# Kernel optimization log

Hardware: AMD Instinct MI355X
Metric: run time of the kernel (lower is better)

Reference implementation:

```python
import jax, jax.numpy as jnp
import numpy as np


def setup_inputs() -> dict:
    key = jax.random.key(0)
    k1, k2 = jax.random.split(key)
    b, c, h, w = 2, 128, 96, 128
    feature0 = jax.random.normal(k1, (b, c, h, w), dtype=jnp.float32)
    feature1 = jax.random.normal(k2, (b, c, h, w), dtype=jnp.float32)
    return {"feature0": feature0, "feature1": feature1, "local_radius": 4}


def reference(feature0, feature1, local_radius):
    # Faithful to the torch module: sample coords are base pixel coords + integer
    # window offsets, so align_corners=True bilinear grid_sample with zeros padding
    # reduces exactly to an integer gather with out-of-bounds masking.
    b, c, h, w = feature0.shape
    r = int(local_radius)
    # base pixel coords (x, y), matching coords_grid channel order
    ys, xs = jnp.meshgrid(jnp.arange(h, dtype=jnp.float32),
                          jnp.arange(w, dtype=jnp.float32), indexing='ij')  # [h,w]
    # window offsets; row-major over (dy, dx) like generate_window_grid reshape(-1,2)
    dy, dx = jnp.meshgrid(jnp.arange(-r, r + 1), jnp.arange(-r, r + 1), indexing='ij')
    dy = dy.reshape(-1).astype(jnp.float32)  # [K]
    dx = dx.reshape(-1).astype(jnp.float32)
    K = dx.shape[0]

    sample_x = xs[:, :, None] + dx  # [h,w,K]
    sample_y = ys[:, :, None] + dy
    valid = ((sample_x >= 0) & (sample_x <= w - 1) &
             (sample_y >= 0) & (sample_y <= h - 1))  # [h,w,K]

    cxi = jnp.clip(sample_x, 0, w - 1).astype(jnp.int32)
    cyi = jnp.clip(sample_y, 0, h - 1).astype(jnp.int32)
    # gather: [b,c,h,w,K]; zeros padding outside bounds
    window_feature = feature1[:, :, cyi, cxi] * valid.astype(feature1.dtype)

    # correlation: per-pixel [1,c] x [c,K]
    corr = jnp.einsum('bchw,bchwk->bhwk', feature0, window_feature) / (c ** 0.5)
    prob = jax.nn.softmax(corr, axis=-1)  # [b,h,w,K]

    # weighted coord sum -> correspondence, then flow = correspondence - coords
    corr_x = jnp.sum(prob * sample_x, axis=-1)  # [b,h,w]
    corr_y = jnp.sum(prob * sample_y, axis=-1)
    flow = jnp.stack([corr_x - xs, corr_y - ys], axis=1)  # [b,2,h,w]

    match_prob = prob.reshape(b, h * w, K)
    return flow, match_prob
```

## Files before the change

kernel.cpp:

```cpp
#include <hip/hip_runtime.h>
#include <math.h>

#define W_ 128
#define H_ 96
#define C_ 128
#define HW_ (H_ * W_)
#define K_ 81
#define FLOW_ELEMS (2 * 2 * H_ * W_)
#define TCOLS 80
#define TSTR 66

typedef __fp16 f16x8 __attribute__((ext_vector_type(8)));
typedef float  f32x4 __attribute__((ext_vector_type(4)));

__device__ __forceinline__ unsigned pack_pair(float a, float b) {
    return __builtin_bit_cast(unsigned, __builtin_amdgcn_cvt_pkrtz(a, b));
}

__global__ __launch_bounds__(256) void fused_kernel(const float* __restrict__ f0,
                                                    const float* __restrict__ f1,
                                                    float* __restrict__ out) {
    __shared__ unsigned tile[TCOLS * TSTR];
    __shared__ float corr_lds[64][85];
    __shared__ float mbuf[64], ibuf[64];
    __shared__ float pmax[4][68], psum[4][68], pfxb[4][68], pfyb[4][68];

    const int t = threadIdx.x;
    const int wid = t >> 6, l = t & 63;
    const int L = (blockIdx.x & 7) * 48 + (blockIdx.x >> 3);
    const int xh = L & 1;
    const int y0 = (L >> 1) % H_;
    const int b  = L / (2 * H_);
    const int px0 = xh * 64 + wid * 16;

    int g_off[5], lds_w[5];
    bool g_ok[5];
#pragma unroll
    for (int i = 0; i < 5; ++i) {
        const int s = i * 256 + t;
        const int cp = s / 20;
        const int q = s - cp * 20;
        const int x0 = xh * 64 + 4 * q - 4;
        g_ok[i] = (x0 >= 0) && (x0 <= 124);
        g_off[i] = 2 * cp * HW_ + (g_ok[i] ? x0 : 0);
        lds_w[i] = (4 * q) * TSTR + cp;
    }
    const float* f1base = f1 + (size_t)b * C_ * HW_;

    f16x8 a[4];
    {
        const float* f0p = f0 + (size_t)b * C_ * HW_ + (size_t)y0 * W_ + px0 + (l & 15);
#pragma unroll
        for (int kk = 0; kk < 4; ++kk) {
            f16x8 av;
#pragma unroll
            for (int j = 0; j < 8; ++j)
                av[j] = (__fp16)f0p[(size_t)(kk * 32 + (l >> 4) * 8 + j) * HW_];
            a[kk] = av;
        }
    }

    auto LOADDY = [&](int dy, float4 (&va)[5], float4 (&vb)[5], bool& ok) {
        const int r = y0 + dy - 4;
        ok = (r >= 0) && (r < H_);
        const float* f1b = f1base + (size_t)(ok ? r : 0) * W_;
#pragma unroll
        for (int i = 0; i < 5; ++i) {
            float4 x = {0.f, 0.f, 0.f, 0.f}, y = {0.f, 0.f, 0.f, 0.f};
            if (ok && g_ok[i]) {
                x = *(const float4*)(f1b + g_off[i]);
                y = *(const float4*)(f1b + g_off[i] + HW_);
            }
            va[i] = x; vb[i] = y;
        }
    };
    auto WRITEDY = [&](const float4 (&va)[5], const float4 (&vb)[5]) {
#pragma unroll
        for (int i = 0; i < 5; ++i) {
            tile[lds_w[i]]            = pack_pair(va[i].x, vb[i].x);
            tile[lds_w[i] + TSTR]     = pack_pair(va[i].y, vb[i].y);
            tile[lds_w[i] + 2 * TSTR] = pack_pair(va[i].z, vb[i].z);
            tile[lds_w[i] + 3 * TSTR] = pack_pair(va[i].w, vb[i].w);
        }
    };
    auto COMPUTE = [&](int dy) {
        f32x4 accA = {0.f, 0.f, 0.f, 0.f}, accB = {0.f, 0.f, 0.f, 0.f};
#pragma unroll
        for (int kk = 0; kk < 4; ++kk) {
            const int off = kk * 16 + (l >> 4) * 4;
            {
                const int col = wid * 16 + (l & 15);
                const uint2 lo = *(const uint2*)&tile[col * TSTR + off];
                const uint2 hi = *(const uint2*)&tile[col * TSTR + off + 2];
                const uint4 u = {lo.x, lo.y, hi.x, hi.y};
                accA = __builtin_amdgcn_mfma_f32_16x16x32_f16(
                    a[kk], __builtin_bit_cast(f16x8, u), accA, 0, 0, 0);
            }
            {
                const int col = wid * 16 + 16 + (l & 15);
                const uint2 lo = *(const uint2*)&tile[col * TSTR + off];
                const uint2 hi = *(const uint2*)&tile[col * TSTR + off + 2];
                const uint4 u = {lo.x, lo.y, hi.x, hi.y};
                accB = __builtin_amdgcn_mfma_f32_16x16x32_f16(
                    a[kk], __builtin_bit_cast(f16x8, u), accB, 0, 0, 0);
            }
        }
#pragma unroll
        for (int h = 0; h < 2; ++h) {
            const f32x4 acc = h ? accB : accA;
#pragma unroll
            for (int rg = 0; rg < 4; ++rg) {
                const int i2 = (l >> 4) * 4 + rg;
                const int j2 = h * 16 + (l & 15);
                const int dxw = j2 - i2;
                if (dxw >= 0 && dxw <= 8)
                    corr_lds[wid * 16 + i2][dy * 9 + dxw] = acc[rg];
            }
        }
    };

    float4 vaA[5], vbA[5], vaB[5], vbB[5], vaC[5], vbC[5];
    bool okA, okB, okC;

    LOADDY(0, vaA, vbA, okA);
    LOADDY(1, vaB, vbB, okB);
    for (int i = t; i < 64 * 85; i += 256) (&corr_lds[0][0])[i] = 0.f;
    __syncthreads();

    if (okA) WRITEDY(vaA, vbA); __syncthreads();
    LOADDY(2, vaC, vbC, okC);
    if (okA) COMPUTE(0); __syncthreads();

    if (okB) WRITEDY(vaB, vbB); __syncthreads();
    LOADDY(3, vaA, vbA, okA);
    if (okB) COMPUTE(1); __syncthreads();

    if (okC) WRITEDY(vaC, vbC); __syncthreads();
    LOADDY(4, vaB, vbB, okB);
    if (okC) COMPUTE(2); __syncthreads();

    if (okA) WRITEDY(vaA, vbA); __syncthreads();
    LOADDY(5, vaC, vbC, okC);
    if (okA) COMPUTE(3); __syncthreads();

    if (okB) WRITEDY(vaB, vbB); __syncthreads();
    LOADDY(6, vaA, vbA, okA);
    if (okB) COMPUTE(4); __syncthreads();

    if (okC) WRITEDY(vaC, vbC); __syncthreads();
    LOADDY(7, vaB, vbB, okB);
    if (okC) COMPUTE(5); __syncthreads();

    if (okA) WRITEDY(vaA, vbA); __syncthreads();
    LOADDY(8, vaC, vbC, okC);
    if (okA) COMPUTE(6); __syncthreads();

    if (okB) WRITEDY(vaB, vbB); __syncthreads();
    if (okB) COMPUTE(7); __syncthreads();

    if (okC) WRITEDY(vaC, vbC); __syncthreads();
    if (okC) COMPUTE(8); __syncthreads();

    const float scale = 0.08838834764831845f;

    {
        const int px = t & 63;
        const int part = t >> 6;
        float pm = -1e30f;
        for (int k = part; k < K_; k += 4)
            pm = fmaxf(pm, corr_lds[px][k] * scale);
        pmax[part][px] = pm;
        __syncthreads();
        const float m = fmaxf(fmaxf(pmax[0][px], pmax[1][px]),
                              fmaxf(pmax[2][px], pmax[3][px]));
        float ps = 0.f, pfx = 0.f, pfy = 0.f;
        for (int k = part; k < K_; k += 4) {
            const float e = __expf(corr_lds[px][k] * scale - m);
            ps += e;
            pfx += e * (float)(k % 9 - 4);
            pfy += e * (float)(k / 9 - 4);
        }
        psum[part][px] = ps; pfxb[part][px] = pfx; pfyb[part][px] = pfy;
        __syncthreads();
        if (t < 64) {
            const float s = psum[0][t] + psum[1][t] + psum[2][t] + psum[3][t];
            const float inv = 1.f / s;
            mbuf[t] = m;
            ibuf[t] = inv;
            const float fx = pfxb[0][t] + pfxb[1][t] + pfxb[2][t] + pfxb[3][t];
            const float fy = pfyb[0][t] + pfyb[1][t] + pfyb[2][t] + pfyb[3][t];
            const int x = xh * 64 + t;
            out[((size_t)(b * 2 + 0) * H_ + y0) * W_ + x] = fx * inv;
            out[((size_t)(b * 2 + 1) * H_ + y0) * W_ + x] = fy * inv;
        }
    }
    __syncthreads();

    float* mp = out + FLOW_ELEMS + ((size_t)b * HW_ + (size_t)y0 * W_ + xh * 64) * K_;
    for (int f = t; f < 64 * K_; f += 256) {
        const int px = f / K_;
        const int k = f - px * K_;
        mp[f] = __expf(corr_lds[px][k] * scale - mbuf[px]) * ibuf[px];
    }
}

extern "C" void kernel_launch(void* const* d_in, const int* in_sizes, int n_in,
                              void* d_out, int out_size, void* d_ws, size_t ws_size,
                              hipStream_t stream) {
    (void)in_sizes; (void)n_in; (void)out_size; (void)d_ws; (void)ws_size;
    const float* f0 = (const float*)d_in[0];
    const float* f1 = (const float*)d_in[1];
    float* out = (float*)d_out;

    fused_kernel<<<384, 256, 0, stream>>>(f0, f1, out);
}
```

Baseline: 27.48 us.

## Split channel reduction across waves with LDS atomics, shrinking pixel tile to 16

Each block now covers 16 pixels instead of 64, and the four waves each take a 32-channel slice of the reduction instead of separate 16-pixel groups. Partial correlations are combined with LDS atomicAdd. The launch grows from 384 to 1536 blocks. The goal is more blocks in flight and a smaller per-block LDS footprint, but each block re-reads an overlapping 24-column f1 halo, uses smaller loads, and pays for shared-memory atomics.

```diff
diff --git a/kernel.cpp b/kernel.cpp
--- a/kernel.cpp
+++ b/kernel.cpp
@@ -7,7 +7,6 @@
 #define HW_ (H_ * W_)
 #define K_ 81
 #define FLOW_ELEMS (2 * 2 * H_ * W_)
-#define TCOLS 80
 #define TSTR 66
 
 typedef __fp16 f16x8 __attribute__((ext_vector_type(8)));
@@ -20,52 +19,48 @@
 __global__ __launch_bounds__(256) void fused_kernel(const float* __restrict__ f0,
                                                     const float* __restrict__ f1,
                                                     float* __restrict__ out) {
-    __shared__ unsigned tile[TCOLS * TSTR];
-    __shared__ float corr_lds[64][85];
-    __shared__ float mbuf[64], ibuf[64];
-    __shared__ float pmax[4][68], psum[4][68], pfxb[4][68], pfyb[4][68];
+    __shared__ unsigned tile[32 * TSTR];
+    __shared__ float corr_lds[16][85];
+    __shared__ float mbuf[16], ibuf[16];
+    __shared__ float pmax[16][17], psum[16][17], pfxb[16][17], pfyb[16][17];
 
     const int t = threadIdx.x;
     const int wid = t >> 6, l = t & 63;
-    const int L = (blockIdx.x & 7) * 48 + (blockIdx.x >> 3);
-    const int xh = L & 1;
-    const int y0 = (L >> 1) % H_;
-    const int b  = L / (2 * H_);
-    const int px0 = xh * 64 + wid * 16;
-
-    int g_off[5], lds_w[5];
-    bool g_ok[5];
-#pragma unroll
-    for (int i = 0; i < 5; ++i) {
+    const int L = (blockIdx.x & 7) * 192 + (blockIdx.x >> 3);
+    const int b = L / 768;
+    const int rem = L - b * 768;
+    const int y0 = rem >> 3;
+    const int xq = rem & 7;
+    const int px0 = xq * 16;
+
+    int g_off[2], lds_w[2];
+    bool g_ok[2];
+#pragma unroll
+    for (int i = 0; i < 2; ++i) {
         const int s = i * 256 + t;
-        const int cp = s / 20;
-        const int q = s - cp * 20;
-        const int x0 = xh * 64 + 4 * q - 4;
+        const int cp = s >> 3;
+        const int q = s & 7;
+        const int x0 = px0 + 4 * q - 4;
         g_ok[i] = (x0 >= 0) && (x0 <= 124);
         g_off[i] = 2 * cp * HW_ + (g_ok[i] ? x0 : 0);
         lds_w[i] = (4 * q) * TSTR + cp;
     }
     const float* f1base = f1 + (size_t)b * C_ * HW_;
 
-    f16x8 a[4];
+    f16x8 a;
     {
         const float* f0p = f0 + (size_t)b * C_ * HW_ + (size_t)y0 * W_ + px0 + (l & 15);
 #pragma unroll
-        for (int kk = 0; kk < 4; ++kk) {
-            f16x8 av;
-#pragma unroll
-            for (int j = 0; j < 8; ++j)
-                av[j] = (__fp16)f0p[(size_t)(kk * 32 + (l >> 4) * 8 + j) * HW_];
-            a[kk] = av;
-        }
-    }
-
-    auto LOADDY = [&](int dy, float4 (&va)[5], float4 (&vb)[5], bool& ok) {
+        for (int j = 0; j < 8; ++j)
+            a[j] = (__fp16)f0p[(size_t)(wid * 32 + (l >> 4) * 8 + j) * HW_];
+    }
+
+    auto LOADDY = [&](int dy, float4 (&va)[2], float4 (&vb)[2], bool& ok) {
         const int r = y0 + dy - 4;
         ok = (r >= 0) && (r < H_);
         const float* f1b = f1base + (size_t)(ok ? r : 0) * W_;
 #pragma unroll
-        for (int i = 0; i < 5; ++i) {
+        for (int i = 0; i < 2; ++i) {
             float4 x = {0.f, 0.f, 0.f, 0.f}, y = {0.f, 0.f, 0.f, 0.f};
             if (ok && g_ok[i]) {
                 x = *(const float4*)(f1b + g_off[i]);
@@ -74,9 +69,9 @@
             va[i] = x; vb[i] = y;
         }
     };
-    auto WRITEDY = [&](const float4 (&va)[5], const float4 (&vb)[5]) {
-#pragma unroll
-        for (int i = 0; i < 5; ++i) {
+    auto WRITEDY = [&](const float4 (&va)[2], const float4 (&vb)[2]) {
+#pragma unroll
+        for (int i = 0; i < 2; ++i) {
             tile[lds_w[i]]            = pack_pair(va[i].x, vb[i].x);
             tile[lds_w[i] + TSTR]     = pack_pair(va[i].y, vb[i].y);
             tile[lds_w[i] + 2 * TSTR] = pack_pair(va[i].z, vb[i].z);
@@ -85,25 +80,22 @@
     };
     auto COMPUTE = [&](int dy) {
         f32x4 accA = {0.f, 0.f, 0.f, 0.f}, accB = {0.f, 0.f, 0.f, 0.f};
-#pragma unroll
-        for (int kk = 0; kk < 4; ++kk) {
-            const int off = kk * 16 + (l >> 4) * 4;
-            {
-                const int col = wid * 16 + (l & 15);
-                const uint2 lo = *(const uint2*)&tile[col * TSTR + off];
-                const uint2 hi = *(const uint2*)&tile[col * TSTR + off + 2];
-                const uint4 u = {lo.x, lo.y, hi.x, hi.y};
-                accA = __builtin_amdgcn_mfma_f32_16x16x32_f16(
-                    a[kk], __builtin_bit_cast(f16x8, u), accA, 0, 0, 0);
-            }
-            {
-                const int col = wid * 16 + 16 + (l & 15);
-                const uint2 lo = *(const uint2*)&tile[col * TSTR + off];
-                const uint2 hi = *(const uint2*)&tile[col * TSTR + off + 2];
-                const uint4 u = {lo.x, lo.y, hi.x, hi.y};
-                accB = __builtin_amdgcn_mfma_f32_16x16x32_f16(
-                    a[kk], __builtin_bit_cast(f16x8, u), accB, 0, 0, 0);
-            }
+        const int off = wid * 16 + (l >> 4) * 4;
+        {
+            const int col = l & 15;
+            const uint2 lo = *(const uint2*)&tile[col * TSTR + off];
+            const uint2 hi = *(const uint2*)&tile[col * TSTR + off + 2];
+            const uint4 u = {lo.x, lo.y, hi.x, hi.y};
+            accA = __builtin_amdgcn_mfma_f32_16x16x32_f16(
+                a, __builtin_bit_cast(f16x8, u), accA, 0, 0, 0);
+        }
+        {
+            const int col = 16 + (l & 15);
+            const uint2 lo = *(const uint2*)&tile[col * TSTR + off];
+            const uint2 hi = *(const uint2*)&tile[col * TSTR + off + 2];
+            const uint4 u = {lo.x, lo.y, hi.x, hi.y};
+            accB = __builtin_amdgcn_mfma_f32_16x16x32_f16(
+                a, __builtin_bit_cast(f16x8, u), accB, 0, 0, 0);
         }
 #pragma unroll
         for (int h = 0; h < 2; ++h) {
@@ -114,17 +106,17 @@
                 const int j2 = h * 16 + (l & 15);
                 const int dxw = j2 - i2;
                 if (dxw >= 0 && dxw <= 8)
-                    corr_lds[wid * 16 + i2][dy * 9 + dxw] = acc[rg];
+                    atomicAdd(&corr_lds[i2][dy * 9 + dxw], acc[rg]);
             }
         }
     };
 
-    float4 vaA[5], vbA[5], vaB[5], vbB[5], vaC[5], vbC[5];
+    float4 vaA[2], vbA[2], vaB[2], vbB[2], vaC[2], vbC[2];
     bool okA, okB, okC;
 
     LOADDY(0, vaA, vbA, okA);
     LOADDY(1, vaB, vbB, okB);
-    for (int i = t; i < 64 * 85; i += 256) (&corr_lds[0][0])[i] = 0.f;
+    for (int i = t; i < 16 * 85; i += 256) (&corr_lds[0][0])[i] = 0.f;
     __syncthreads();
 
     if (okA) WRITEDY(vaA, vbA); __syncthreads();
@@ -164,17 +156,19 @@
     const float scale = 0.08838834764831845f;
 
     {
-        const int px = t & 63;
-        const int part = t >> 6;
+        const int px = t & 15;
+        const int part = t >> 4;
         float pm = -1e30f;
-        for (int k = part; k < K_; k += 4)
+        for (int k = part; k < K_; k += 16)
             pm = fmaxf(pm, corr_lds[px][k] * scale);
         pmax[part][px] = pm;
         __syncthreads();
-        const float m = fmaxf(fmaxf(pmax[0][px], pmax[1][px]),
-                              fmaxf(pmax[2][px], pmax[3][px]));
+        float m = -1e30f;
+#pragma unroll
+        for (int p = 0; p < 16; ++p) m = fmaxf(m, pmax[p][px]);
+        if (part == 0) mbuf[px] = m;
         float ps = 0.f, pfx = 0.f, pfy = 0.f;
-        for (int k = part; k < K_; k += 4) {
+        for (int k = part; k < K_; k += 16) {
             const float e = __expf(corr_lds[px][k] * scale - m);
             ps += e;
             pfx += e * (float)(k % 9 - 4);
@@ -182,22 +176,23 @@
         }
         psum[part][px] = ps; pfxb[part][px] = pfx; pfyb[part][px] = pfy;
         __syncthreads();
-        if (t < 64) {
-            const float s = psum[0][t] + psum[1][t] + psum[2][t] + psum[3][t];
+        if (t < 16) {
+            float s = 0.f, fx = 0.f, fy = 0.f;
+#pragma unroll
+            for (int p = 0; p < 16; ++p) {
+                s += psum[p][t]; fx += pfxb[p][t]; fy += pfyb[p][t];
+            }
             const float inv = 1.f / s;
-            mbuf[t] = m;
             ibuf[t] = inv;
-            const float fx = pfxb[0][t] + pfxb[1][t] + pfxb[2][t] + pfxb[3][t];
-            const float fy = pfyb[0][t] + pfyb[1][t] + pfyb[2][t] + pfyb[3][t];
-            const int x = xh * 64 + t;
+            const int x = px0 + t;
             out[((size_t)(b * 2 + 0) * H_ + y0) * W_ + x] = fx * inv;
             out[((size_t)(b * 2 + 1) * H_ + y0) * W_ + x] = fy * inv;
         }
     }
     __syncthreads();
 
-    float* mp = out + FLOW_ELEMS + ((size_t)b * HW_ + (size_t)y0 * W_ + xh * 64) * K_;
-    for (int f = t; f < 64 * K_; f += 256) {
+    float* mp = out + FLOW_ELEMS + ((size_t)b * HW_ + (size_t)y0 * W_ + px0) * K_;
+    for (int f = t; f < 16 * K_; f += 256) {
         const int px = f / K_;
         const int k = f - px * K_;
         mp[f] = __expf(corr_lds[px][k] * scale - mbuf[px]) * ibuf[px];
@@ -212,5 +207,5 @@
     const float* f1 = (const float*)d_in[1];
     float* out = (float*)d_out;
 
-    fused_kernel<<<384, 256, 0, stream>>>(f0, f1, out);
+    fused_kernel<<<1536, 256, 0, stream>>>(f0, f1, out);
 }
```

Result: slower. 57.40 us (+108.9%).

## Process two dy rows per stage with double LDS tile to halve barriers

Applied to the files above, without the earlier changes.

The nine-row loop over window offsets is restructured to stage two f1 rows per step into two LDS tile slots, then compute both dy values before the next barrier. This halves the number of __syncthreads rounds and issues twice as many global loads per prefetch. In exchange it doubles the LDS tile footprint and raises register pressure, since four pairs of float4 arrays are now held in flight, which may reduce occupancy.

```diff
diff --git a/kernel.cpp b/kernel.cpp
--- a/kernel.cpp
+++ b/kernel.cpp
@@ -20,7 +20,7 @@
 __global__ __launch_bounds__(256) void fused_kernel(const float* __restrict__ f0,
                                                     const float* __restrict__ f1,
                                                     float* __restrict__ out) {
-    __shared__ unsigned tile[TCOLS * TSTR];
+    __shared__ unsigned tile2[2][TCOLS * TSTR];
     __shared__ float corr_lds[64][85];
     __shared__ float mbuf[64], ibuf[64];
     __shared__ float pmax[4][68], psum[4][68], pfxb[4][68], pfyb[4][68];
@@ -60,46 +60,57 @@
         }
     }
 
-    auto LOADDY = [&](int dy, float4 (&va)[5], float4 (&vb)[5], bool& ok) {
-        const int r = y0 + dy - 4;
-        ok = (r >= 0) && (r < H_);
-        const float* f1b = f1base + (size_t)(ok ? r : 0) * W_;
+    auto LOADPAIR = [&](int p, float4 (&va)[5], float4 (&vb)[5],
+                        float4 (&wa)[5], float4 (&wb)[5], bool& ok0, bool& ok1) {
+        const int r0 = y0 + 2 * p - 4;
+        const int r1 = r0 + 1;
+        ok0 = (r0 >= 0) && (r0 < H_);
+        ok1 = (2 * p + 1 <= 8) && (r1 >= 0) && (r1 < H_);
+        const float* fb0 = f1base + (size_t)(ok0 ? r0 : 0) * W_;
+        const float* fb1 = f1base + (size_t)(ok1 ? r1 : 0) * W_;
 #pragma unroll
         for (int i = 0; i < 5; ++i) {
-            float4 x = {0.f, 0.f, 0.f, 0.f}, y = {0.f, 0.f, 0.f, 0.f};
-            if (ok && g_ok[i]) {
-                x = *(const float4*)(f1b + g_off[i]);
-                y = *(const float4*)(f1b + g_off[i] + HW_);
-            }
-            va[i] = x; vb[i] = y;
+            float4 x0v = {0.f, 0.f, 0.f, 0.f}, y0v = {0.f, 0.f, 0.f, 0.f};
+            float4 x1v = {0.f, 0.f, 0.f, 0.f}, y1v = {0.f, 0.f, 0.f, 0.f};
+            if (ok0 && g_ok[i]) {
+                x0v = *(const float4*)(fb0 + g_off[i]);
+                y0v = *(const float4*)(fb0 + g_off[i] + HW_);
+            }
+            if (ok1 && g_ok[i]) {
+                x1v = *(const float4*)(fb1 + g_off[i]);
+                y1v = *(const float4*)(fb1 + g_off[i] + HW_);
+            }
+            va[i] = x0v; vb[i] = y0v; wa[i] = x1v; wb[i] = y1v;
         }
     };
-    auto WRITEDY = [&](const float4 (&va)[5], const float4 (&vb)[5]) {
+    auto WRITEROW = [&](int slot, const float4 (&va)[5], const float4 (&vb)[5]) {
+        unsigned* tl = tile2[slot];
 #pragma unroll
         for (int i = 0; i < 5; ++i) {
-            tile[lds_w[i]]            = pack_pair(va[i].x, vb[i].x);
-            tile[lds_w[i] + TSTR]     = pack_pair(va[i].y, vb[i].y);
-            tile[lds_w[i] + 2 * TSTR] = pack_pair(va[i].z, vb[i].z);
-            tile[lds_w[i] + 3 * TSTR] = pack_pair(va[i].w, vb[i].w);
+            tl[lds_w[i]]            = pack_pair(va[i].x, vb[i].x);
+            tl[lds_w[i] + TSTR]     = pack_pair(va[i].y, vb[i].y);
+            tl[lds_w[i] + 2 * TSTR] = pack_pair(va[i].z, vb[i].z);
+            tl[lds_w[i] + 3 * TSTR] = pack_pair(va[i].w, vb[i].w);
         }
     };
     auto COMPUTE = [&](int dy) {
+        const unsigned* tl = tile2[dy & 1];
         f32x4 accA = {0.f, 0.f, 0.f, 0.f}, accB = {0.f, 0.f, 0.f, 0.f};
 #pragma unroll
         for (int kk = 0; kk < 4; ++kk) {
             const int off = kk * 16 + (l >> 4) * 4;
             {
                 const int col = wid * 16 + (l & 15);
-                const uint2 lo = *(const uint2*)&tile[col * TSTR + off];
-                const uint2 hi = *(const uint2*)&tile[col * TSTR + off + 2];
+                const uint2 lo = *(const uint2*)&tl[col * TSTR + off];
+                const uint2 hi = *(const uint2*)&tl[col * TSTR + off + 2];
                 const uint4 u = {lo.x, lo.y, hi.x, hi.y};
                 accA = __builtin_amdgcn_mfma_f32_16x16x32_f16(
                     a[kk], __builtin_bit_cast(f16x8, u), accA, 0, 0, 0);
             }
             {
                 const int col = wid * 16 + 16 + (l & 15);
-                const uint2 lo = *(const uint2*)&tile[col * TSTR + off];
-                const uint2 hi = *(const uint2*)&tile[col * TSTR + off + 2];
+                const uint2 lo = *(const uint2*)&tl[col * TSTR + off];
+                const uint2 hi = *(const uint2*)&tl[col * TSTR + off + 2];
                 const uint4 u = {lo.x, lo.y, hi.x, hi.y};
                 accB = __builtin_amdgcn_mfma_f32_16x16x32_f16(
                     a[kk], __builtin_bit_cast(f16x8, u), accB, 0, 0, 0);
@@ -119,47 +130,65 @@
         }
     };
 
-    float4 vaA[5], vbA[5], vaB[5], vbB[5], vaC[5], vbC[5];
-    bool okA, okB, okC;
-
-    LOADDY(0, vaA, vbA, okA);
-    LOADDY(1, vaB, vbB, okB);
+    float4 vaA[5], vbA[5], waA[5], wbA[5];
+    float4 vaB[5], vbB[5], waB[5], wbB[5];
+    bool okA0, okA1, okB0, okB1;
+
+    LOADPAIR(0, vaA, vbA, waA, wbA, okA0, okA1);
+    LOADPAIR(1, vaB, vbB, waB, wbB, okB0, okB1);
     for (int i = t; i < 64 * 85; i += 256) (&corr_lds[0][0])[i] = 0.f;
     __syncthreads();
 
-    if (okA) WRITEDY(vaA, vbA); __syncthreads();
-    LOADDY(2, vaC, vbC, okC);
-    if (okA) COMPUTE(0); __syncthreads();
-
-    if (okB) WRITEDY(vaB, vbB); __syncthreads();
-    LOADDY(3, vaA, vbA, okA);
-    if (okB) COMPUTE(1); __syncthreads();
-
-    if (okC) WRITEDY(vaC, vbC); __syncthreads();
-    LOADDY(4, vaB, vbB, okB);
-    if (okC) COMPUTE(2); __syncthreads();
-
-    if (okA) WRITEDY(vaA, vbA); __syncthreads();
-    LOADDY(5, vaC, vbC, okC);
-    if (okA) COMPUTE(3); __syncthreads();
-
-    if (okB) WRITEDY(vaB, vbB); __syncthreads();
-    LOADDY(6, vaA, vbA, okA);
-    if (okB) COMPUTE(4); __syncthreads();
-
-    if (okC) WRITEDY(vaC, vbC); __syncthreads();
-    LOADDY(7, vaB, vbB, okB);
-    if (okC) COMPUTE(5); __syncthreads();
-
-    if (okA) WRITEDY(vaA, vbA); __syncthreads();
-    LOADDY(8, vaC, vbC, okC);
-    if (okA) COMPUTE(6); __syncthreads();
-
-    if (okB) WRITEDY(vaB, vbB); __syncthreads();
-    if (okB) COMPUTE(7); __syncthreads();
-
-    if (okC) WRITEDY(vaC, vbC); __syncthreads();
-    if (okC) COMPUTE(8); __syncthreads();
+    if (okA0) WRITEROW(0, vaA, vbA);
+    if (okA1) WRITEROW(1, waA, wbA);
+    __syncthreads();
+    LOADPAIR(2, vaA, vbA, waA, wbA, okA0, okA1);
+    {
+        const int r0 = y0 + 0 - 4, r1 = r0 + 1;
+        if (r0 >= 0 && r0 < H_) COMPUTE(0);
+        if (r1 >= 0 && r1 < H_) COMPUTE(1);
+    }
+    __syncthreads();
+
+    if (okB0) WRITEROW(0, vaB, vbB);
+    if (okB1) WRITEROW(1, waB, wbB);
+    __syncthreads();
+    LOADPAIR(3, vaB, vbB, waB, wbB, okB0, okB1);
+    {
+        const int r0 = y0 + 2 - 4, r1 = r0 + 1;
+        if (r0 >= 0 && r0 < H_) COMPUTE(2);
+        if (r1 >= 0 && r1 < H_) COMPUTE(3);
+    }
+    __syncthreads();
+
+    if (okA0) WRITEROW(0, vaA, vbA);
+    if (okA1) WRITEROW(1, waA, wbA);
+    __syncthreads();
+    LOADPAIR(4, vaA, vbA, waA, wbA, okA0, okA1);
+    {
+        const int r0 = y0 + 4 - 4, r1 = r0 + 1;
+        COMPUTE(4);
+        if (r1 >= 0 && r1 < H_) COMPUTE(5);
+    }
+    __syncthreads();
+
+    if (okB0) WRITEROW(0, vaB, vbB);
+    if (okB1) WRITEROW(1, waB, wbB);
+    __syncthreads();
+    {
+        const int r0 = y0 + 6 - 4, r1 = r0 + 1;
+        if (r0 >= 0 && r0 < H_) COMPUTE(6);
+        if (r1 >= 0 && r1 < H_) COMPUTE(7);
+    }
+    __syncthreads();
+
+    if (okA0) WRITEROW(0, vaA, vbA);
+    __syncthreads();
+    {
+        const int r0 = y0 + 8 - 4;
+        if (r0 >= 0 && r0 < H_) COMPUTE(8);
+    }
+    __syncthreads();
 
     const float scale = 0.08838834764831845f;
 
```

Result: no change. 27.73 us (+0.9%).

## Tile 3 rows x 32 cols per block to reuse feature1 rows across rows

Applied to the files above, without the earlier changes.

Each block now handles a 3-row by 32-column output tile with 6 waves. Every loaded feature1 row is shared by up to three output rows, so a block streams 11 rows instead of 9 per output row, which cuts redundant global loads of feature1. The softmax scale is folded into feature0 before the fp16 conversion, and the exponentials are cached in LDS so they are not recomputed in the output pass. In exchange the grid drops to 256 blocks of 384 threads and uses more LDS and more phases, and rows 32 columns wide mean more halo overhead per load.

```diff
diff --git a/kernel.cpp b/kernel.cpp
--- a/kernel.cpp
+++ b/kernel.cpp
@@ -7,7 +7,7 @@
 #define HW_ (H_ * W_)
 #define K_ 81
 #define FLOW_ELEMS (2 * 2 * H_ * W_)
-#define TCOLS 80
+#define TCOLS 48
 #define TSTR 66
 
 typedef __fp16 f16x8 __attribute__((ext_vector_type(8)));
@@ -17,55 +17,60 @@
     return __builtin_bit_cast(unsigned, __builtin_amdgcn_cvt_pkrtz(a, b));
 }
 
-__global__ __launch_bounds__(256) void fused_kernel(const float* __restrict__ f0,
+__global__ __launch_bounds__(384) void fused_kernel(const float* __restrict__ f0,
                                                     const float* __restrict__ f1,
                                                     float* __restrict__ out) {
     __shared__ unsigned tile[TCOLS * TSTR];
-    __shared__ float corr_lds[64][85];
-    __shared__ float mbuf[64], ibuf[64];
-    __shared__ float pmax[4][68], psum[4][68], pfxb[4][68], pfyb[4][68];
+    __shared__ float corr_lds[3][32][85];
+    __shared__ float pmax[4][96], psum[4][96], pfxb[4][96], pfyb[4][96];
+    __shared__ float ibuf[96];
 
     const int t = threadIdx.x;
     const int wid = t >> 6, l = t & 63;
-    const int L = (blockIdx.x & 7) * 48 + (blockIdx.x >> 3);
-    const int xh = L & 1;
-    const int y0 = (L >> 1) % H_;
-    const int b  = L / (2 * H_);
-    const int px0 = xh * 64 + wid * 16;
-
-    int g_off[5], lds_w[5];
-    bool g_ok[5];
-#pragma unroll
-    for (int i = 0; i < 5; ++i) {
-        const int s = i * 256 + t;
-        const int cp = s / 20;
-        const int q = s - cp * 20;
-        const int x0 = xh * 64 + 4 * q - 4;
+    const int ry = wid >> 1, xt = wid & 1;
+    const int L = (blockIdx.x & 7) * 32 + (blockIdx.x >> 3);
+    const int b = L >> 7;
+    const int rem = L & 127;
+    const int ys = rem >> 2, xq = rem & 3;
+    const int y0 = ys * 3;
+    const int px0 = xq * 32;
+    const int pxw = px0 + xt * 16;
+
+    int g_off[2], lds_w[2];
+    bool g_ok[2];
+#pragma unroll
+    for (int i = 0; i < 2; ++i) {
+        const int s = i * 384 + t;
+        const int cp = s / 12;
+        const int q = s - cp * 12;
+        const int x0 = px0 + 4 * q - 4;
         g_ok[i] = (x0 >= 0) && (x0 <= 124);
         g_off[i] = 2 * cp * HW_ + (g_ok[i] ? x0 : 0);
         lds_w[i] = (4 * q) * TSTR + cp;
     }
     const float* f1base = f1 + (size_t)b * C_ * HW_;
 
+    const float scale = 0.08838834764831845f;
     f16x8 a[4];
     {
-        const float* f0p = f0 + (size_t)b * C_ * HW_ + (size_t)y0 * W_ + px0 + (l & 15);
+        const float* f0p = f0 + (size_t)b * C_ * HW_ + (size_t)(y0 + ry) * W_
+                              + pxw + (l & 15);
 #pragma unroll
         for (int kk = 0; kk < 4; ++kk) {
             f16x8 av;
 #pragma unroll
             for (int j = 0; j < 8; ++j)
-                av[j] = (__fp16)f0p[(size_t)(kk * 32 + (l >> 4) * 8 + j) * HW_];
+                av[j] = (__fp16)(f0p[(size_t)(kk * 32 + (l >> 4) * 8 + j) * HW_] * scale);
             a[kk] = av;
         }
     }
 
-    auto LOADDY = [&](int dy, float4 (&va)[5], float4 (&vb)[5], bool& ok) {
-        const int r = y0 + dy - 4;
+    auto LOADP = [&](int p, float4 (&va)[2], float4 (&vb)[2], bool& ok) {
+        const int r = y0 - 4 + p;
         ok = (r >= 0) && (r < H_);
         const float* f1b = f1base + (size_t)(ok ? r : 0) * W_;
 #pragma unroll
-        for (int i = 0; i < 5; ++i) {
+        for (int i = 0; i < 2; ++i) {
             float4 x = {0.f, 0.f, 0.f, 0.f}, y = {0.f, 0.f, 0.f, 0.f};
             if (ok && g_ok[i]) {
                 x = *(const float4*)(f1b + g_off[i]);
@@ -74,22 +79,22 @@
             va[i] = x; vb[i] = y;
         }
     };
-    auto WRITEDY = [&](const float4 (&va)[5], const float4 (&vb)[5]) {
-#pragma unroll
-        for (int i = 0; i < 5; ++i) {
+    auto WRITEP = [&](const float4 (&va)[2], const float4 (&vb)[2]) {
+#pragma unroll
+        for (int i = 0; i < 2; ++i) {
             tile[lds_w[i]]            = pack_pair(va[i].x, vb[i].x);
             tile[lds_w[i] + TSTR]     = pack_pair(va[i].y, vb[i].y);
             tile[lds_w[i] + 2 * TSTR] = pack_pair(va[i].z, vb[i].z);
             tile[lds_w[i] + 3 * TSTR] = pack_pair(va[i].w, vb[i].w);
         }
     };
-    auto COMPUTE = [&](int dy) {
+    auto COMPUTE = [&](int dyi) {
         f32x4 accA = {0.f, 0.f, 0.f, 0.f}, accB = {0.f, 0.f, 0.f, 0.f};
 #pragma unroll
         for (int kk = 0; kk < 4; ++kk) {
             const int off = kk * 16 + (l >> 4) * 4;
             {
-                const int col = wid * 16 + (l & 15);
+                const int col = xt * 16 + (l & 15);
                 const uint2 lo = *(const uint2*)&tile[col * TSTR + off];
                 const uint2 hi = *(const uint2*)&tile[col * TSTR + off + 2];
                 const uint4 u = {lo.x, lo.y, hi.x, hi.y};
@@ -97,7 +102,7 @@
                     a[kk], __builtin_bit_cast(f16x8, u), accA, 0, 0, 0);
             }
             {
-                const int col = wid * 16 + 16 + (l & 15);
+                const int col = xt * 16 + 16 + (l & 15);
                 const uint2 lo = *(const uint2*)&tile[col * TSTR + off];
                 const uint2 hi = *(const uint2*)&tile[col * TSTR + off + 2];
                 const uint4 u = {lo.x, lo.y, hi.x, hi.y};
@@ -114,93 +119,85 @@
                 const int j2 = h * 16 + (l & 15);
                 const int dxw = j2 - i2;
                 if (dxw >= 0 && dxw <= 8)
-                    corr_lds[wid * 16 + i2][dy * 9 + dxw] = acc[rg];
+                    corr_lds[ry][xt * 16 + i2][dyi * 9 + dxw] = acc[rg];
             }
         }
     };
 
-    float4 vaA[5], vbA[5], vaB[5], vbB[5], vaC[5], vbC[5];
+    float4 vaA[2], vbA[2], vaB[2], vbB[2], vaC[2], vbC[2];
     bool okA, okB, okC;
 
-    LOADDY(0, vaA, vbA, okA);
-    LOADDY(1, vaB, vbB, okB);
-    for (int i = t; i < 64 * 85; i += 256) (&corr_lds[0][0])[i] = 0.f;
+    LOADP(0, vaA, vbA, okA);
+    LOADP(1, vaB, vbB, okB);
+    for (int i = t; i < 3 * 32 * 85; i += 384) (&corr_lds[0][0][0])[i] = 0.f;
     __syncthreads();
 
-    if (okA) WRITEDY(vaA, vbA); __syncthreads();
-    LOADDY(2, vaC, vbC, okC);
-    if (okA) COMPUTE(0); __syncthreads();
-
-    if (okB) WRITEDY(vaB, vbB); __syncthreads();
-    LOADDY(3, vaA, vbA, okA);
-    if (okB) COMPUTE(1); __syncthreads();
-
-    if (okC) WRITEDY(vaC, vbC); __syncthreads();
-    LOADDY(4, vaB, vbB, okB);
-    if (okC) COMPUTE(2); __syncthreads();
-
-    if (okA) WRITEDY(vaA, vbA); __syncthreads();
-    LOADDY(5, vaC, vbC, okC);
-    if (okA) COMPUTE(3); __syncthreads();
-
-    if (okB) WRITEDY(vaB, vbB); __syncthreads();
-    LOADDY(6, vaA, vbA, okA);
-    if (okB) COMPUTE(4); __syncthreads();
-
-    if (okC) WRITEDY(vaC, vbC); __syncthreads();
-    LOADDY(7, vaB, vbB, okB);
-    if (okC) COMPUTE(5); __syncthreads();
-
-    if (okA) WRITEDY(vaA, vbA); __syncthreads();
-    LOADDY(8, vaC, vbC, okC);
-    if (okA) COMPUTE(6); __syncthreads();
-
-    if (okB) WRITEDY(vaB, vbB); __syncthreads();
-    if (okB) COMPUTE(7); __syncthreads();
-
-    if (okC) WRITEDY(vaC, vbC); __syncthreads();
-    if (okC) COMPUTE(8); __syncthreads();
-
-    const float scale = 0.08838834764831845f;
+#define PHASE(p, VA, VB, OK, LP, NVA, NVB, NOK)                              \
+    do {                                                                     \
+        if (OK) WRITEP(VA, VB);                                              \
+        __syncthreads();                                                     \
+        if (LP <= 10) LOADP(LP, NVA, NVB, NOK);                              \
+        const int dyi = (p) - ry;                                            \
+        if (OK && dyi >= 0 && dyi <= 8) COMPUTE(dyi);                        \
+        __syncthreads();                                                     \
+    } while (0)
+
+    PHASE(0, vaA, vbA, okA, 2, vaC, vbC, okC);
+    PHASE(1, vaB, vbB, okB, 3, vaA, vbA, okA);
+    PHASE(2, vaC, vbC, okC, 4, vaB, vbB, okB);
+    PHASE(3, vaA, vbA, okA, 5, vaC, vbC, okC);
+    PHASE(4, vaB, vbB, okB, 6, vaA, vbA, okA);
+    PHASE(5, vaC, vbC, okC, 7, vaB, vbB, okB);
+    PHASE(6, vaA, vbA, okA, 8, vaC, vbC, okC);
+    PHASE(7, vaB, vbB, okB, 9, vaA, vbA, okA);
+    PHASE(8, vaC, vbC, okC, 10, vaB, vbB, okB);
+    PHASE(9, vaA, vbA, okA, 11, vaC, vbC, okC);
+    PHASE(10, vaB, vbB, okB, 11, vaC, vbC, okC);
+#undef PHASE
 
     {
-        const int px = t & 63;
-        const int part = t >> 6;
+        const int pxi = t % 96;
+        const int part = t / 96;
+        const int sry = pxi >> 5, spx = pxi & 31;
         float pm = -1e30f;
         for (int k = part; k < K_; k += 4)
-            pm = fmaxf(pm, corr_lds[px][k] * scale);
-        pmax[part][px] = pm;
+            pm = fmaxf(pm, corr_lds[sry][spx][k]);
+        pmax[part][pxi] = pm;
         __syncthreads();
-        const float m = fmaxf(fmaxf(pmax[0][px], pmax[1][px]),
-                              fmaxf(pmax[2][px], pmax[3][px]));
+        const float m = fmaxf(fmaxf(pmax[0][pxi], pmax[1][pxi]),
+                              fmaxf(pmax[2][pxi], pmax[3][pxi]));
         float ps = 0.f, pfx = 0.f, pfy = 0.f;
         for (int k = part; k < K_; k += 4) {
-            const float e = __expf(corr_lds[px][k] * scale - m);
+            const float e = __expf(corr_lds[sry][spx][k] - m);
+            corr_lds[sry][spx][k] = e;
             ps += e;
             pfx += e * (float)(k % 9 - 4);
             pfy += e * (float)(k / 9 - 4);
         }
-        psum[part][px] = ps; pfxb[part][px] = pfx; pfyb[part][px] = pfy;
+        psum[part][pxi] = ps; pfxb[part][pxi] = pfx; pfyb[part][pxi] = pfy;
         __syncthreads();
-        if (t < 64) {
+        if (t < 96) {
             const float s = psum[0][t] + psum[1][t] + psum[2][t] + psum[3][t];
             const float inv = 1.f / s;
-            mbuf[t] = m;
             ibuf[t] = inv;
             const float fx = pfxb[0][t] + pfxb[1][t] + pfxb[2][t] + pfxb[3][t];
             const float fy = pfyb[0][t] + pfyb[1][t] + pfyb[2][t] + pfyb[3][t];
-            const int x = xh * 64 + t;
-            out[((size_t)(b * 2 + 0) * H_ + y0) * W_ + x] = fx * inv;
-            out[((size_t)(b * 2 + 1) * H_ + y0) * W_ + x] = fy * inv;
+            const int yy = y0 + (t >> 5);
+            const int x = px0 + (t & 31);
+            out[((size_t)(b * 2 + 0) * H_ + yy) * W_ + x] = fx * inv;
+            out[((size_t)(b * 2 + 1) * H_ + yy) * W_ + x] = fy * inv;
         }
     }
     __syncthreads();
 
-    float* mp = out + FLOW_ELEMS + ((size_t)b * HW_ + (size_t)y0 * W_ + xh * 64) * K_;
-    for (int f = t; f < 64 * K_; f += 256) {
-        const int px = f / K_;
-        const int k = f - px * K_;
-        mp[f] = __expf(corr_lds[px][k] * scale - mbuf[px]) * ibuf[px];
+    float* outp = out + FLOW_ELEMS;
+    for (int f = t; f < 96 * K_; f += 384) {
+        const int pxi = f / K_;
+        const int k = f - pxi * K_;
+        const int yy = y0 + (pxi >> 5);
+        const int x = px0 + (pxi & 31);
+        outp[((size_t)b * HW_ + (size_t)yy * W_ + x) * K_ + k] =
+            corr_lds[pxi >> 5][pxi & 31][k] * ibuf[pxi];
     }
 }
 
@@ -212,5 +209,5 @@
     const float* f1 = (const float*)d_in[1];
     float* out = (float*)d_out;
 
-    fused_kernel<<<384, 256, 0, stream>>>(f0, f1, out);
+    fused_kernel<<<256, 384, 0, stream>>>(f0, f1, out);
 }
```

After: 23.82 us. -13.3%, faster.
